# Optimization experiments

Measured on AMD Instinct MI355X. Metric: run time of the kernel, lower is better.

## Reference

```python
import jax, jax.numpy as jnp
import numpy as np

N_NODES = 50000   # field_size == number of graph nodes
N_EDGES = 800000  # avg degree 16
VOCAB = 200000    # feature_size
EMB = 64          # embedding_size == in_dim
HID = 64          # num_hidden
SLOPE = 0.2       # leaky relu negative slope


def setup_inputs() -> dict:
    key = jax.random.key(0)
    ks = jax.random.split(key, 20)
    s = 0.05
    d = {}
    d["features"] = jax.random.randint(ks[0], (8, N_NODES), 0, VOCAB, dtype=jnp.int32)
    d["feature_values"] = jax.random.uniform(ks[1], (8, N_NODES), dtype=jnp.float32)
    d["src"] = jax.random.randint(ks[2], (N_EDGES,), 0, N_NODES, dtype=jnp.int32)
    d["dst"] = jax.random.randint(ks[3], (N_EDGES,), 0, N_NODES, dtype=jnp.int32)
    d["emb"] = jax.random.normal(ks[4], (VOCAB, EMB), jnp.float32) * s
    # layer 0: in=64 -> heads=2, out=64 (no residual)
    d["W0"]  = jax.random.normal(ks[5], (EMB, 2 * HID), jnp.float32) * s
    d["al0"] = jax.random.normal(ks[6], (2, HID), jnp.float32) * s
    d["ar0"] = jax.random.normal(ks[7], (2, HID), jnp.float32) * s
    d["b0"]  = jnp.zeros((2 * HID,), jnp.float32)
    # layer 1: in=128 -> heads=2, out=64 (identity residual since in == heads*out)
    d["W1"]  = jax.random.normal(ks[8], (2 * HID, 2 * HID), jnp.float32) * s
    d["al1"] = jax.random.normal(ks[9], (2, HID), jnp.float32) * s
    d["ar1"] = jax.random.normal(ks[10], (2, HID), jnp.float32) * s
    d["b1"]  = jnp.zeros((2 * HID,), jnp.float32)
    # output layer: in=128 -> heads=1, out=64 (projected residual), no activation
    d["W2"]    = jax.random.normal(ks[11], (2 * HID, EMB), jnp.float32) * s
    d["al2"]   = jax.random.normal(ks[12], (1, EMB), jnp.float32) * s
    d["ar2"]   = jax.random.normal(ks[13], (1, EMB), jnp.float32) * s
    d["b2"]    = jnp.zeros((EMB,), jnp.float32)
    d["resW2"] = jax.random.normal(ks[14], (2 * HID, EMB), jnp.float32) * s
    return d


def _gat_layer(h, src, dst, W, al, ar, b, res, act):
    """DGL-style GATConv. h: [N, in], W: [in, H*D], al/ar: [H, D]."""
    N = h.shape[0]
    H, D = al.shape
    fh = (h @ W).reshape(N, H, D)                      # [N, H, D]
    el = jnp.einsum('nhd,hd->nh', fh, al)              # [N, H]
    er = jnp.einsum('nhd,hd->nh', fh, ar)              # [N, H]
    e = jax.nn.leaky_relu(el[src] + er[dst], SLOPE)    # [E, H]
    # edge softmax grouped by destination node
    m = jax.ops.segment_max(e, dst, num_segments=N)
    m = jnp.where(jnp.isfinite(m), m, 0.0)
    ex = jnp.exp(e - m[dst])
    den = jax.ops.segment_sum(ex, dst, num_segments=N)
    alpha = ex / jnp.maximum(den[dst], 1e-9)           # [E, H]
    out = jax.ops.segment_sum(alpha[:, :, None] * fh[src], dst, num_segments=N)  # [N, H, D]
    if res is not None:
        out = out + res
    out = out + b.reshape(H, D)
    if act:
        out = jax.nn.elu(out)
    return out


def reference(features, feature_values, src, dst, emb,
              W0, al0, ar0, b0, W1, al1, ar1, b1,
              W2, al2, ar2, b2, resW2):
    # embedding lookup scaled by feature values: [B, field, emb]
    fe = emb[features] * feature_values[..., None]
    h = fe[0]                                          # [N_NODES, EMB]
    # layer 0: no residual, elu, flatten heads
    h = _gat_layer(h, src, dst, W0, al0, ar0, b0, None, True).reshape(N_NODES, -1)
    # layer 1: identity residual (in == heads*out), elu, flatten heads
    res1 = h.reshape(N_NODES, 2, HID)
    h = _gat_layer(h, src, dst, W1, al1, ar1, b1, res1, True).reshape(N_NODES, -1)
    # output layer: projected residual, no activation, mean over heads
    res2 = (h @ resW2).reshape(N_NODES, 1, EMB)
    logits = _gat_layer(h, src, dst, W2, al2, ar2, b2, res2, False).mean(axis=1)
    return logits
```

## Files before the change

kernel.cpp:

```cpp
#include <hip/hip_runtime.h>


typedef __attribute__((ext_vector_type(8))) short short8;
typedef __attribute__((ext_vector_type(4))) float float4v;

__device__ __forceinline__ float lrelu(float x){ return fmaxf(x, 0.2f*x); }

__device__ __forceinline__ unsigned short f2bf(float f){
  unsigned int u = __float_as_uint(f);
  u += 0x7fffu + ((u >> 16) & 1u);
  return (unsigned short)(u >> 16);
}
__device__ __forceinline__ float bf2f(unsigned short u){
  return __uint_as_float((unsigned int)u << 16);
}
__device__ __forceinline__ float rl_f(float v, int l){
  return __int_as_float(__builtin_amdgcn_readlane(__float_as_int(v), l));
}

__global__ void k_zero_i32(int* __restrict__ p, int n){
  int i = blockIdx.x*blockDim.x + threadIdx.x;
  if (i < n) p[i] = 0;
}

__global__ void k_hist_rank(const int* __restrict__ dst, int* __restrict__ counts,
                            int* __restrict__ rank, int E){
  int i = blockIdx.x*blockDim.x + threadIdx.x;
  if (i < E){
    int d = dst[i];
    rank[i] = atomicAdd(&counts[d], 1);
  }
}

__global__ void k_scan_local(const int* __restrict__ counts, int* __restrict__ row_ptr,
                             int* __restrict__ bsum, int N){
  __shared__ int s[256];
  int t = threadIdx.x, g = blockIdx.x*256 + t;
  int v = (g < N) ? counts[g] : 0;
  s[t] = v; __syncthreads();
  #pragma unroll
  for (int off = 1; off < 256; off <<= 1){
    int x = 0;
    if (t >= off) x = s[t-off];
    __syncthreads();
    s[t] += x;
    __syncthreads();
  }
  if (g < N) row_ptr[g+1] = s[t];
  if (g == 0 && t == 0) row_ptr[0] = 0;
  if (t == 255) bsum[blockIdx.x] = s[255];
}

__global__ void k_scan_top(int* __restrict__ bsum, int nb){
  __shared__ int s[256];
  int t = threadIdx.x;
  int v = (t < nb) ? bsum[t] : 0;
  s[t] = v; __syncthreads();
  #pragma unroll
  for (int off = 1; off < 256; off <<= 1){
    int x = 0;
    if (t >= off) x = s[t-off];
    __syncthreads();
    s[t] += x;
    __syncthreads();
  }
  if (t < nb) bsum[t] = s[t] - v;
}

__global__ void k_scan_fix(int* __restrict__ row_ptr, const int* __restrict__ bsum, int N){
  int g = blockIdx.x*256 + threadIdx.x;
  if (g < N && blockIdx.x > 0) row_ptr[g+1] += bsum[blockIdx.x];
}

__global__ void k_scatter2(const int* __restrict__ src, const int* __restrict__ dst,
                           const int* __restrict__ rank, const int* __restrict__ row_ptr,
                           int* __restrict__ ssrc, int E){
  int i = blockIdx.x*blockDim.x + threadIdx.x;
  if (i < E) ssrc[row_ptr[dst[i]] + rank[i]] = src[i];
}

__global__ void k_wprep_all(const float* __restrict__ W0, const float* __restrict__ W1,
                            const float* __restrict__ W2, const float* __restrict__ rW2,
                            unsigned short* __restrict__ Wt0, unsigned short* __restrict__ Wt1,
                            unsigned short* __restrict__ Wt2){
  int id = blockIdx.x*256 + threadIdx.x;
  if (id < 128*64){
    int n = id/64, k = id%64;
    Wt0[n*64 + k] = f2bf(W0[k*128 + n]);
  } else if (id < 128*64 + 128*128){
    int i = id - 128*64; int n = i/128, k = i%128;
    Wt1[n*128 + k] = f2bf(W1[k*128 + n]);
  } else if (id < 128*64 + 2*128*128){
    int i = id - 128*64 - 128*128; int n = i/128, k = i%128;
    float v = (n < 64) ? W2[k*64 + n] : rW2[k*64 + (n - 64)];
    Wt2[n*128 + k] = f2bf(v);
  }
}

__global__ void k_embed(const int* __restrict__ feat, const float* __restrict__ fv,
                        const float* __restrict__ emb, unsigned int* __restrict__ h0b, int N){
  int t = blockIdx.x*blockDim.x + threadIdx.x;
  int n = t >> 4, c4 = t & 15;
  if (n >= N) return;
  float4 v = ((const float4*)(emb + (size_t)feat[n]*64))[c4];
  float sc = fv[n];
  unsigned int p0 = (unsigned)f2bf(v.x*sc) | ((unsigned)f2bf(v.y*sc) << 16);
  unsigned int p1 = (unsigned)f2bf(v.z*sc) | ((unsigned)f2bf(v.w*sc) << 16);
  h0b[(size_t)n*32 + c4*2]     = p0;
  h0b[(size_t)n*32 + c4*2 + 1] = p1;
}

template<int IN, int H>
__global__ __launch_bounds__(256) void k_gemm_mfma(
    const unsigned short* __restrict__ hb,
    const unsigned short* __restrict__ Wt,
    const float* __restrict__ al, const float* __restrict__ ar,
    unsigned short* __restrict__ fhb,
    float* __restrict__ elr, int N){
  constexpr int KS = IN/32;
  constexpr int LDP = IN + 8;
  __shared__ unsigned short Wt_s[128*LDP];
  const int t = threadIdx.x;
  const int lane = t & 63, wid = t >> 6;
  const int l15 = lane & 15, quad = lane >> 4;
  const int row0 = blockIdx.x*64 + wid*16;

  for (int id = t; id < 128*(IN/8); id += 256){
    int r = id/(IN/8), seg = id%(IN/8);
    ((uint4*)(Wt_s + r*LDP))[seg] = ((const uint4*)(Wt + (size_t)r*IN))[seg];
  }
  short8 a[KS];
  int arow = row0 + l15;
  #pragma unroll
  for (int s = 0; s < KS; s++){
    if (arow < N) a[s] = *(const short8*)(hb + (size_t)arow*IN + s*32 + quad*8);
    else          a[s] = short8{0,0,0,0,0,0,0,0};
  }
  __syncthreads();

  float4v acc[8];
  #pragma unroll
  for (int nt = 0; nt < 8; nt++) acc[nt] = float4v{0.f,0.f,0.f,0.f};
  #pragma unroll
  for (int nt = 0; nt < 8; nt++){
    #pragma unroll
    for (int s = 0; s < KS; s++){
      short8 b = *(const short8*)(Wt_s + (nt*16 + l15)*LDP + s*32 + quad*8);
      acc[nt] = __builtin_amdgcn_mfma_f32_16x16x32_bf16(a[s], b, acc[nt], 0, 0, 0);
    }
  }

  float alc[8], arc[8];
  #pragma unroll
  for (int nt = 0; nt < 8; nt++){
    bool hv = (H == 2) || (nt < 4);
    alc[nt] = hv ? al[nt*16 + l15] : 0.f;
    arc[nt] = hv ? ar[nt*16 + l15] : 0.f;
  }
  #pragma unroll
  for (int reg = 0; reg < 4; reg++){
    int row = row0 + quad*4 + reg;
    bool rv = row < N;
    if (rv){
      #pragma unroll
      for (int nt = 0; nt < 8; nt++)
        fhb[(size_t)row*128 + nt*16 + l15] = f2bf(acc[nt][reg]);
    }
    float pel0 = 0.f, per0 = 0.f, pel1 = 0.f, per1 = 0.f;
    #pragma unroll
    for (int nt = 0; nt < 4; nt++){
      pel0 += acc[nt][reg]*alc[nt];     per0 += acc[nt][reg]*arc[nt];
      pel1 += acc[nt+4][reg]*alc[nt+4]; per1 += acc[nt+4][reg]*arc[nt+4];
    }
    #pragma unroll
    for (int off = 1; off < 16; off <<= 1){
      pel0 += __shfl_xor(pel0, off, 64);
      pel1 += __shfl_xor(pel1, off, 64);
      per0 += __shfl_xor(per0, off, 64);
      per1 += __shfl_xor(per1, off, 64);
    }
    if (l15 == 0 && rv){
      elr[row*4+0] = pel0;
      elr[row*4+1] = (H == 2) ? pel1 : 0.f;
      elr[row*4+2] = per0;
      elr[row*4+3] = (H == 2) ? per1 : 0.f;
    }
  }
}

template<int H>
__global__ __launch_bounds__(256) void k_agg(
    const unsigned* __restrict__ fhb, const float* __restrict__ elr,
    const int* __restrict__ row_ptr, const int* __restrict__ ssrc,
    const float* __restrict__ bias, const float* __restrict__ res,
    int act, int res_from_fh,
    float* __restrict__ out, int out_ld, unsigned* __restrict__ outb, int N){
  int lane = threadIdx.x & 63, wid = threadIdx.x >> 6;
  int n = blockIdx.x*4 + wid;
  if (n >= N) return;
  int beg = row_ptr[n], end = row_ptr[n+1];
  float er0 = elr[n*4+2];
  float er1 = (H == 2) ? elr[n*4+3] : 0.f;

  float x0 = 0.f, x1 = 0.f;
  {
    int i = beg + lane;
    if (i < end){
      int s = ssrc[i];
      float2 el = *(const float2*)(elr + s*4);
      x0 = __expf(fminf(lrelu(el.x + er0), 30.f));
      if (H == 2) x1 = __expf(fminf(lrelu(el.y + er1), 30.f));
    }
  }
  float d0 = x0, d1 = x1;
  for (int i = beg + lane + 64; i < end; i += 64){
    int s = ssrc[i];
    float2 el = *(const float2*)(elr + s*4);
    d0 += __expf(fminf(lrelu(el.x + er0), 30.f));
    if (H == 2) d1 += __expf(fminf(lrelu(el.y + er1), 30.f));
  }
  #pragma unroll
  for (int off = 32; off >= 1; off >>= 1){
    d0 += __shfl_xor(d0, off, 64);
    if (H == 2) d1 += __shfl_xor(d1, off, 64);
  }
  float rd0 = d0 > 0.f ? 1.f/d0 : 0.f;
  float rd1 = (H == 2 && d1 > 0.f) ? 1.f/d1 : 0.f;

  float ax = 0.f, ay = 0.f;
  const int idxbase = (lane & 32) << 2;
  for (int base = beg; base < end; base += 64){
    int i = base + lane;
    int s = 0; float a0 = 0.f, a1 = 0.f;
    if (i < end){
      s = ssrc[i];
      if (base == beg){
        a0 = x0 * rd0; if (H == 2) a1 = x1 * rd1;
      } else {
        float2 el = *(const float2*)(elr + s*4);
        a0 = __expf(fminf(lrelu(el.x + er0), 30.f)) * rd0;
        if (H == 2) a1 = __expf(fminf(lrelu(el.y + er1), 30.f)) * rd1;
      }
    }
    int cnt  = min(64, end - base);
    int cnt8 = (cnt + 7) & ~7;
    if (H == 2){
      float a1x = __shfl_xor(a1, 32, 64);
      float a0x = __shfl_xor(a0, 32, 64);
      int ap  = __float_as_int((lane < 32) ? a0  : a1x);
      int ap2 = __float_as_int((lane < 32) ? a0x : a1);
      for (int j0 = 0; j0 < cnt8; j0 += 8){
        int apx = (j0 < 32) ? ap : ap2;
        int jb = j0 & 31;
        unsigned w[8]; float aj[8];
        #pragma unroll
        for (int u = 0; u < 8; u++){
          int sj = __builtin_amdgcn_readlane(s, j0 + u);
          w[u] = fhb[(size_t)sj*64 + lane];
        }
        #pragma unroll
        for (int u = 0; u < 8; u++)
          aj[u] = __int_as_float(
              __builtin_amdgcn_ds_bpermute(idxbase + ((jb + u) << 2), apx));
        #pragma unroll
        for (int u = 0; u < 8; u++){
          ax += bf2f((unsigned short)(w[u] & 0xffffu)) * aj[u];
          ay += bf2f((unsigned short)(w[u] >> 16))     * aj[u];
        }
      }
    } else {
      const unsigned short* fh16 = (const unsigned short*)fhb;
      for (int j0 = 0; j0 < cnt8; j0 += 8){
        unsigned short w[8]; float aj[8];
        #pragma unroll
        for (int u = 0; u < 8; u++){
          int sj = __builtin_amdgcn_readlane(s, j0 + u);
          w[u] = fh16[(size_t)sj*128 + lane];
        }
        #pragma unroll
        for (int u = 0; u < 8; u++) aj[u] = rl_f(a0, j0 + u);
        #pragma unroll
        for (int u = 0; u < 8; u++) ax += bf2f(w[u]) * aj[u];
      }
    }
  }
  if (H == 2){
    int c0 = lane*2;
    float o0 = ax + bias[c0], o1 = ay + bias[c0+1];
    if (res){ o0 += res[n*128 + c0]; o1 += res[n*128 + c0+1]; }
    if (act){ o0 = o0 > 0.f ? o0 : expm1f(o0); o1 = o1 > 0.f ? o1 : expm1f(o1); }
    if (out) *(float2*)(out + n*out_ld + c0) = make_float2(o0, o1);
    if (outb) outb[(size_t)n*64 + lane] = (unsigned)f2bf(o0) | ((unsigned)f2bf(o1) << 16);
  } else {
    const unsigned short* fh16 = (const unsigned short*)fhb;
    float o = ax + bias[lane];
    if (res_from_fh) o += bf2f(fh16[(size_t)n*128 + 64 + lane]);
    out[n*out_ld + lane] = o;
  }
}

extern "C" void kernel_launch(void* const* d_in, const int* in_sizes, int n_in,
                              void* d_out, int out_size, void* d_ws, size_t ws_size,
                              hipStream_t stream) {
  const int*   feat = (const int*)  d_in[0];
  const float* fv   = (const float*)d_in[1];
  const int*   src  = (const int*)  d_in[2];
  const int*   dst  = (const int*)  d_in[3];
  const float* emb  = (const float*)d_in[4];
  const float* W0   = (const float*)d_in[5];
  const float* al0  = (const float*)d_in[6];
  const float* ar0  = (const float*)d_in[7];
  const float* b0   = (const float*)d_in[8];
  const float* W1   = (const float*)d_in[9];
  const float* al1  = (const float*)d_in[10];
  const float* ar1  = (const float*)d_in[11];
  const float* b1   = (const float*)d_in[12];
  const float* W2   = (const float*)d_in[13];
  const float* al2  = (const float*)d_in[14];
  const float* ar2  = (const float*)d_in[15];
  const float* b2   = (const float*)d_in[16];
  const float* rW2  = (const float*)d_in[17];
  const int N = in_sizes[0] / 8;
  const int E = in_sizes[2];

  size_t off = 0;
  auto alloc = [&](size_t bytes) -> void* {
    void* p = (char*)d_ws + off;
    off = (off + bytes + 255) & ~(size_t)255;
    return p;
  };
  unsigned short* P1 = (unsigned short*)alloc((size_t)N*128*sizeof(unsigned short));
  float* P2     = (float*)alloc((size_t)N*128*sizeof(float));
  unsigned short* hb = (unsigned short*)alloc((size_t)N*128*sizeof(unsigned short));
  float* elr    = (float*)alloc((size_t)N*4*sizeof(float));
  int* row_ptr  = (int*)alloc((size_t)(N+1)*sizeof(int));
  int* counts   = (int*)alloc((size_t)N*sizeof(int));
  int* rank     = (int*)alloc((size_t)E*sizeof(int));
  int* ssrc     = (int*)alloc((size_t)E*sizeof(int));
  int* bsum     = (int*)alloc(256*sizeof(int));
  unsigned short* Wt0 = (unsigned short*)alloc((size_t)128*64*sizeof(unsigned short));
  unsigned short* Wt1 = (unsigned short*)alloc((size_t)128*128*sizeof(unsigned short));
  unsigned short* Wt2 = (unsigned short*)alloc((size_t)128*128*sizeof(unsigned short));

  int nb1 = (N + 255) / 256;
  k_zero_i32<<<(N + 255)/256, 256, 0, stream>>>(counts, N);
  k_hist_rank<<<(E + 255)/256, 256, 0, stream>>>(dst, counts, rank, E);
  k_scan_local<<<nb1, 256, 0, stream>>>(counts, row_ptr, bsum, N);
  k_scan_top<<<1, 256, 0, stream>>>(bsum, nb1);
  k_scan_fix<<<nb1, 256, 0, stream>>>(row_ptr, bsum, N);
  k_scatter2<<<(E + 255)/256, 256, 0, stream>>>(src, dst, rank, row_ptr, ssrc, E);
  k_wprep_all<<<(128*64 + 2*128*128 + 255)/256, 256, 0, stream>>>(
      W0, W1, W2, rW2, Wt0, Wt1, Wt2);
  k_embed<<<(N*16 + 255)/256, 256, 0, stream>>>(feat, fv, emb, (unsigned int*)hb, N);

  int gt = (N + 63)/64;
  int nagg = (N + 3)/4;
  k_gemm_mfma<64,2><<<gt, 256, 0, stream>>>(hb, Wt0, al0, ar0, P1, elr, N);
  k_agg<2><<<nagg, 256, 0, stream>>>((unsigned*)P1, elr, row_ptr, ssrc, b0, nullptr,
                                     1, 0, P2, 128, (unsigned*)hb, N);
  k_gemm_mfma<128,2><<<gt, 256, 0, stream>>>(hb, Wt1, al1, ar1, P1, elr, N);
  k_agg<2><<<nagg, 256, 0, stream>>>((unsigned*)P1, elr, row_ptr, ssrc, b1, P2,
                                     1, 0, nullptr, 128, (unsigned*)hb, N);
  k_gemm_mfma<128,1><<<gt, 256, 0, stream>>>(hb, Wt2, al2, ar2, P1, elr, N);
  k_agg<1><<<nagg, 256, 0, stream>>>((unsigned*)P1, elr, row_ptr, ssrc, b2, nullptr,
                                     0, 1, (float*)d_out, 64, nullptr, N);
}
```

Measured before the change: 333.1 us.

## Vectorize aggregation gathers with 16-byte fp16 loads and fuse embedding into GEMM

The aggregation kernel switches from one 4-byte gather per lane per edge to 16-byte loads. Lane groups each handle a different edge, and partial sums are reduced across groups with shuffles at the end. Features are now stored as fp16 instead of bf16, which gives more mantissa precision and allows packed half2 conversion. The embedding lookup and scaling move into the first GEMM kernel, dropping one launch and the intermediate store and reload of h0. The trade-offs are the extra cross-lane reduction work and fp16 range limits on the stored features.

```diff
diff --git a/kernel.cpp b/kernel.cpp
--- a/kernel.cpp
+++ b/kernel.cpp
@@ -1,4 +1,5 @@
 #include <hip/hip_runtime.h>
+#include <hip/hip_fp16.h>
 
 
 typedef __attribute__((ext_vector_type(8))) short short8;
@@ -11,11 +12,18 @@
   u += 0x7fffu + ((u >> 16) & 1u);
   return (unsigned short)(u >> 16);
 }
-__device__ __forceinline__ float bf2f(unsigned short u){
-  return __uint_as_float((unsigned int)u << 16);
-}
-__device__ __forceinline__ float rl_f(float v, int l){
-  return __int_as_float(__builtin_amdgcn_readlane(__float_as_int(v), l));
+__device__ __forceinline__ unsigned short f2h(float f){
+  return __half_as_ushort(__float2half(f));
+}
+__device__ __forceinline__ float2 h2f2(unsigned v){
+  __half2 h = *reinterpret_cast<__half2*>(&v);
+  return __half22float2(h);
+}
+__device__ __forceinline__ int bperm(int idx, int v){
+  return __builtin_amdgcn_ds_bpermute(idx, v);
+}
+__device__ __forceinline__ float bperm_f(int idx, int v){
+  return __int_as_float(__builtin_amdgcn_ds_bpermute(idx, v));
 }
 
 __global__ void k_zero_i32(int* __restrict__ p, int n){
@@ -97,22 +105,11 @@
   }
 }
 
-__global__ void k_embed(const int* __restrict__ feat, const float* __restrict__ fv,
-                        const float* __restrict__ emb, unsigned int* __restrict__ h0b, int N){
-  int t = blockIdx.x*blockDim.x + threadIdx.x;
-  int n = t >> 4, c4 = t & 15;
-  if (n >= N) return;
-  float4 v = ((const float4*)(emb + (size_t)feat[n]*64))[c4];
-  float sc = fv[n];
-  unsigned int p0 = (unsigned)f2bf(v.x*sc) | ((unsigned)f2bf(v.y*sc) << 16);
-  unsigned int p1 = (unsigned)f2bf(v.z*sc) | ((unsigned)f2bf(v.w*sc) << 16);
-  h0b[(size_t)n*32 + c4*2]     = p0;
-  h0b[(size_t)n*32 + c4*2 + 1] = p1;
-}
-
-template<int IN, int H>
+template<int IN, int H, bool EMBED>
 __global__ __launch_bounds__(256) void k_gemm_mfma(
     const unsigned short* __restrict__ hb,
+    const int* __restrict__ feat, const float* __restrict__ fv,
+    const float* __restrict__ embp,
     const unsigned short* __restrict__ Wt,
     const float* __restrict__ al, const float* __restrict__ ar,
     unsigned short* __restrict__ fhb,
@@ -131,10 +128,31 @@
   }
   short8 a[KS];
   int arow = row0 + l15;
-  #pragma unroll
-  for (int s = 0; s < KS; s++){
-    if (arow < N) a[s] = *(const short8*)(hb + (size_t)arow*IN + s*32 + quad*8);
-    else          a[s] = short8{0,0,0,0,0,0,0,0};
+  if (EMBED){
+    if (arow < N){
+      const float* er2 = embp + (size_t)feat[arow]*64;
+      float sc = fv[arow];
+      #pragma unroll
+      for (int s = 0; s < KS; s++){
+        const float4* p = (const float4*)(er2 + s*32 + quad*8);
+        float4 v0 = p[0], v1 = p[1];
+        short8 ta;
+        ta[0] = (short)f2bf(v0.x*sc); ta[1] = (short)f2bf(v0.y*sc);
+        ta[2] = (short)f2bf(v0.z*sc); ta[3] = (short)f2bf(v0.w*sc);
+        ta[4] = (short)f2bf(v1.x*sc); ta[5] = (short)f2bf(v1.y*sc);
+        ta[6] = (short)f2bf(v1.z*sc); ta[7] = (short)f2bf(v1.w*sc);
+        a[s] = ta;
+      }
+    } else {
+      #pragma unroll
+      for (int s = 0; s < KS; s++) a[s] = short8{0,0,0,0,0,0,0,0};
+    }
+  } else {
+    #pragma unroll
+    for (int s = 0; s < KS; s++){
+      if (arow < N) a[s] = *(const short8*)(hb + (size_t)arow*IN + s*32 + quad*8);
+      else          a[s] = short8{0,0,0,0,0,0,0,0};
+    }
   }
   __syncthreads();
 
@@ -164,7 +182,7 @@
     if (rv){
       #pragma unroll
       for (int nt = 0; nt < 8; nt++)
-        fhb[(size_t)row*128 + nt*16 + l15] = f2bf(acc[nt][reg]);
+        fhb[(size_t)row*128 + nt*16 + l15] = f2h(acc[nt][reg]);
     }
     float pel0 = 0.f, per0 = 0.f, pel1 = 0.f, per1 = 0.f;
     #pragma unroll
@@ -190,7 +208,8 @@
 
 template<int H>
 __global__ __launch_bounds__(256) void k_agg(
-    const unsigned* __restrict__ fhb, const float* __restrict__ elr,
+    const unsigned short* __restrict__ fhb,
+    const float* __restrict__ elr,
     const int* __restrict__ row_ptr, const int* __restrict__ ssrc,
     const float* __restrict__ bias, const float* __restrict__ res,
     int act, int res_from_fh,
@@ -203,11 +222,12 @@
   float er1 = (H == 2) ? elr[n*4+3] : 0.f;
 
   float x0 = 0.f, x1 = 0.f;
+  int s_first = 0;
   {
     int i = beg + lane;
     if (i < end){
-      int s = ssrc[i];
-      float2 el = *(const float2*)(elr + s*4);
+      s_first = ssrc[i];
+      float2 el = *(const float2*)(elr + s_first*4);
       x0 = __expf(fminf(lrelu(el.x + er0), 30.f));
       if (H == 2) x1 = __expf(fminf(lrelu(el.y + er1), 30.f));
     }
@@ -227,75 +247,132 @@
   float rd0 = d0 > 0.f ? 1.f/d0 : 0.f;
   float rd1 = (H == 2 && d1 > 0.f) ? 1.f/d1 : 0.f;
 
-  float ax = 0.f, ay = 0.f;
-  const int idxbase = (lane & 32) << 2;
+  const uint4* fh4 = (const uint4*)fhb;
+  const int g = (H == 2) ? (lane >> 4) : (lane >> 3);
+  const int c = (H == 2) ? (lane & 15) : (lane & 7);
+  const int head32 = (H == 2 && c >= 8) ? 32 : 0;
+  float acc[8];
+  #pragma unroll
+  for (int k = 0; k < 8; k++) acc[k] = 0.f;
+
   for (int base = beg; base < end; base += 64){
-    int i = base + lane;
     int s = 0; float a0 = 0.f, a1 = 0.f;
-    if (i < end){
-      s = ssrc[i];
-      if (base == beg){
-        a0 = x0 * rd0; if (H == 2) a1 = x1 * rd1;
-      } else {
-        float2 el = *(const float2*)(elr + s*4);
-        a0 = __expf(fminf(lrelu(el.x + er0), 30.f)) * rd0;
-        if (H == 2) a1 = __expf(fminf(lrelu(el.y + er1), 30.f)) * rd1;
-      }
-    }
-    int cnt  = min(64, end - base);
-    int cnt8 = (cnt + 7) & ~7;
+    {
+      int i = base + lane;
+      if (i < end){
+        if (base == beg){
+          s = s_first;
+          a0 = x0 * rd0; if (H == 2) a1 = x1 * rd1;
+        } else {
+          s = ssrc[i];
+          float2 el = *(const float2*)(elr + s*4);
+          a0 = __expf(fminf(lrelu(el.x + er0), 30.f)) * rd0;
+          if (H == 2) a1 = __expf(fminf(lrelu(el.y + er1), 30.f)) * rd1;
+        }
+      }
+    }
+    int cnt = min(64, end - base);
     if (H == 2){
       float a1x = __shfl_xor(a1, 32, 64);
       float a0x = __shfl_xor(a0, 32, 64);
       int ap  = __float_as_int((lane < 32) ? a0  : a1x);
       int ap2 = __float_as_int((lane < 32) ? a0x : a1);
-      for (int j0 = 0; j0 < cnt8; j0 += 8){
+      for (int j0 = 0; j0 < cnt; j0 += 8){
         int apx = (j0 < 32) ? ap : ap2;
         int jb = j0 & 31;
-        unsigned w[8]; float aj[8];
-        #pragma unroll
-        for (int u = 0; u < 8; u++){
-          int sj = __builtin_amdgcn_readlane(s, j0 + u);
-          w[u] = fhb[(size_t)sj*64 + lane];
+        int sj[2]; uint4 w[2]; float aj[2];
+        #pragma unroll
+        for (int u = 0; u < 2; u++) sj[u] = bperm((j0 + 4*u + g) << 2, s);
+        #pragma unroll
+        for (int u = 0; u < 2; u++) w[u] = fh4[(size_t)(unsigned)sj[u]*16 + c];
+        #pragma unroll
+        for (int u = 0; u < 2; u++) aj[u] = bperm_f((head32 + jb + 4*u + g) << 2, apx);
+        #pragma unroll
+        for (int u = 0; u < 2; u++){
+          const unsigned* wp = (const unsigned*)&w[u];
+          #pragma unroll
+          for (int q = 0; q < 4; q++){
+            float2 f = h2f2(wp[q]);
+            acc[2*q]   = fmaf(f.x, aj[u], acc[2*q]);
+            acc[2*q+1] = fmaf(f.y, aj[u], acc[2*q+1]);
+          }
         }
-        #pragma unroll
-        for (int u = 0; u < 8; u++)
-          aj[u] = __int_as_float(
-              __builtin_amdgcn_ds_bpermute(idxbase + ((jb + u) << 2), apx));
-        #pragma unroll
-        for (int u = 0; u < 8; u++){
-          ax += bf2f((unsigned short)(w[u] & 0xffffu)) * aj[u];
-          ay += bf2f((unsigned short)(w[u] >> 16))     * aj[u];
+      }
+    } else {
+      int av = __float_as_int(a0);
+      for (int j0 = 0; j0 < cnt; j0 += 8){
+        int sj = bperm((j0 + g) << 2, s);
+        uint4 w = fh4[(size_t)(unsigned)sj*16 + c];
+        float aj = bperm_f((j0 + g) << 2, av);
+        const unsigned* wp = (const unsigned*)&w;
+        #pragma unroll
+        for (int q = 0; q < 4; q++){
+          float2 f = h2f2(wp[q]);
+          acc[2*q]   = fmaf(f.x, aj, acc[2*q]);
+          acc[2*q+1] = fmaf(f.y, aj, acc[2*q+1]);
         }
       }
-    } else {
-      const unsigned short* fh16 = (const unsigned short*)fhb;
-      for (int j0 = 0; j0 < cnt8; j0 += 8){
-        unsigned short w[8]; float aj[8];
-        #pragma unroll
-        for (int u = 0; u < 8; u++){
-          int sj = __builtin_amdgcn_readlane(s, j0 + u);
-          w[u] = fh16[(size_t)sj*128 + lane];
+    }
+  }
+
+  #pragma unroll
+  for (int k = 0; k < 8; k++){
+    if (H == 1) acc[k] += __shfl_xor(acc[k], 8, 64);
+    acc[k] += __shfl_xor(acc[k], 16, 64);
+    acc[k] += __shfl_xor(acc[k], 32, 64);
+  }
+
+  if (H == 2){
+    if (lane < 16){
+      int cc = lane;
+      float o[8];
+      const float4* b4 = (const float4*)bias;
+      float4 ba = b4[cc*2], bb = b4[cc*2+1];
+      o[0]=acc[0]+ba.x; o[1]=acc[1]+ba.y; o[2]=acc[2]+ba.z; o[3]=acc[3]+ba.w;
+      o[4]=acc[4]+bb.x; o[5]=acc[5]+bb.y; o[6]=acc[6]+bb.z; o[7]=acc[7]+bb.w;
+      if (res){
+        const float4* r4 = (const float4*)(res + (size_t)n*128);
+        float4 ra = r4[cc*2], rb = r4[cc*2+1];
+        o[0]+=ra.x; o[1]+=ra.y; o[2]+=ra.z; o[3]+=ra.w;
+        o[4]+=rb.x; o[5]+=rb.y; o[6]+=rb.z; o[7]+=rb.w;
+      }
+      if (act){
+        #pragma unroll
+        for (int k = 0; k < 8; k++) o[k] = o[k] > 0.f ? o[k] : expm1f(o[k]);
+      }
+      if (out){
+        float4* o4 = (float4*)(out + (size_t)n*out_ld);
+        o4[cc*2]   = make_float4(o[0], o[1], o[2], o[3]);
+        o4[cc*2+1] = make_float4(o[4], o[5], o[6], o[7]);
+      }
+      if (outb){
+        uint4 ob;
+        ob.x = (unsigned)f2bf(o[0]) | ((unsigned)f2bf(o[1]) << 16);
+        ob.y = (unsigned)f2bf(o[2]) | ((unsigned)f2bf(o[3]) << 16);
+        ob.z = (unsigned)f2bf(o[4]) | ((unsigned)f2bf(o[5]) << 16);
+        ob.w = (unsigned)f2bf(o[6]) | ((unsigned)f2bf(o[7]) << 16);
+        *(uint4*)(outb + (size_t)n*64 + cc*4) = ob;
+      }
+    }
+  } else {
+    if (lane < 8){
+      int cc = lane;
+      float o[8];
+      #pragma unroll
+      for (int k = 0; k < 8; k++) o[k] = acc[k] + bias[cc*8 + k];
+      if (res_from_fh){
+        uint4 r = fh4[(size_t)n*16 + 8 + cc];
+        const unsigned* rp = (const unsigned*)&r;
+        #pragma unroll
+        for (int q = 0; q < 4; q++){
+          float2 f = h2f2(rp[q]);
+          o[2*q] += f.x; o[2*q+1] += f.y;
         }
-        #pragma unroll
-        for (int u = 0; u < 8; u++) aj[u] = rl_f(a0, j0 + u);
-        #pragma unroll
-        for (int u = 0; u < 8; u++) ax += bf2f(w[u]) * aj[u];
-      }
-    }
-  }
-  if (H == 2){
-    int c0 = lane*2;
-    float o0 = ax + bias[c0], o1 = ay + bias[c0+1];
-    if (res){ o0 += res[n*128 + c0]; o1 += res[n*128 + c0+1]; }
-    if (act){ o0 = o0 > 0.f ? o0 : expm1f(o0); o1 = o1 > 0.f ? o1 : expm1f(o1); }
-    if (out) *(float2*)(out + n*out_ld + c0) = make_float2(o0, o1);
-    if (outb) outb[(size_t)n*64 + lane] = (unsigned)f2bf(o0) | ((unsigned)f2bf(o1) << 16);
-  } else {
-    const unsigned short* fh16 = (const unsigned short*)fhb;
-    float o = ax + bias[lane];
-    if (res_from_fh) o += bf2f(fh16[(size_t)n*128 + 64 + lane]);
-    out[n*out_ld + lane] = o;
+      }
+      float4* o4 = (float4*)(out + (size_t)n*out_ld);
+      o4[cc*2]   = make_float4(o[0], o[1], o[2], o[3]);
+      o4[cc*2+1] = make_float4(o[4], o[5], o[6], o[7]);
+    }
   }
 }
 
@@ -351,17 +428,19 @@
   k_scatter2<<<(E + 255)/256, 256, 0, stream>>>(src, dst, rank, row_ptr, ssrc, E);
   k_wprep_all<<<(128*64 + 2*128*128 + 255)/256, 256, 0, stream>>>(
       W0, W1, W2, rW2, Wt0, Wt1, Wt2);
-  k_embed<<<(N*16 + 255)/256, 256, 0, stream>>>(feat, fv, emb, (unsigned int*)hb, N);
 
   int gt = (N + 63)/64;
   int nagg = (N + 3)/4;
-  k_gemm_mfma<64,2><<<gt, 256, 0, stream>>>(hb, Wt0, al0, ar0, P1, elr, N);
-  k_agg<2><<<nagg, 256, 0, stream>>>((unsigned*)P1, elr, row_ptr, ssrc, b0, nullptr,
+  k_gemm_mfma<64,2,true><<<gt, 256, 0, stream>>>(nullptr, feat, fv, emb,
+                                                 Wt0, al0, ar0, P1, elr, N);
+  k_agg<2><<<nagg, 256, 0, stream>>>(P1, elr, row_ptr, ssrc, b0, nullptr,
                                      1, 0, P2, 128, (unsigned*)hb, N);
-  k_gemm_mfma<128,2><<<gt, 256, 0, stream>>>(hb, Wt1, al1, ar1, P1, elr, N);
-  k_agg<2><<<nagg, 256, 0, stream>>>((unsigned*)P1, elr, row_ptr, ssrc, b1, P2,
+  k_gemm_mfma<128,2,false><<<gt, 256, 0, stream>>>(hb, nullptr, nullptr, nullptr,
+                                                   Wt1, al1, ar1, P1, elr, N);
+  k_agg<2><<<nagg, 256, 0, stream>>>(P1, elr, row_ptr, ssrc, b1, P2,
                                      1, 0, nullptr, 128, (unsigned*)hb, N);
-  k_gemm_mfma<128,1><<<gt, 256, 0, stream>>>(hb, Wt2, al2, ar2, P1, elr, N);
-  k_agg<1><<<nagg, 256, 0, stream>>>((unsigned*)P1, elr, row_ptr, ssrc, b2, nullptr,
+  k_gemm_mfma<128,1,false><<<gt, 256, 0, stream>>>(hb, nullptr, nullptr, nullptr,
+                                                   Wt2, al2, ar2, P1, elr, N);
+  k_agg<1><<<nagg, 256, 0, stream>>>(P1, elr, row_ptr, ssrc, b2, nullptr,
                                      0, 1, (float*)d_out, 64, nullptr, N);
 }
```

Measured after the change: 335.1 us. About the same (+0.6%).
